# Kernel optimization log

Hardware: AMD Instinct MI355X
Metric: run time of the kernel (lower is better)

## Reference

```python
import jax, jax.numpy as jnp
import numpy as np

B, N, C = 8, 1024, 768
H, D = 12, 64
SCALE = D ** -0.5
EPS = 1e-5

def layernorm(x, g, b):
    mu = jnp.mean(x, axis=-1, keepdims=True)
    var = jnp.var(x, axis=-1, keepdims=True)
    return (x - mu) * jax.lax.rsqrt(var + EPS) * g + b

def setup_inputs() -> dict:
    key = jax.random.key(0)
    ks = jax.random.split(key, 5)
    return {
        "x": jax.random.normal(ks[0], (B, N, C), jnp.float32),
        "qkv_w": jax.random.normal(ks[1], (3 * C, C), jnp.float32) * 0.02,
        "qkv_b": jax.random.normal(ks[2], (3 * C,), jnp.float32) * 0.02,
        "qn_g": jnp.ones((D,), jnp.float32),
        "qn_b": jnp.zeros((D,), jnp.float32),
        "kn_g": jnp.ones((D,), jnp.float32),
        "kn_b": jnp.zeros((D,), jnp.float32),
        "proj_w": jax.random.normal(ks[3], (C, C), jnp.float32) * 0.02,
        "proj_b": jnp.zeros((C,), jnp.float32),
    }

def reference(x, qkv_w, qkv_b, qn_g, qn_b, kn_g, kn_b, proj_w, proj_b):
    # qkv projection: [B,N,3C] -> [3,B,H,N,D]
    qkv = jnp.einsum('bnc,oc->bno', x, qkv_w) + qkv_b
    qkv = qkv.reshape(B, N, 3, H, D).transpose(2, 0, 3, 1, 4)
    q, k, v = qkv[0], qkv[1], qkv[2]
    q = layernorm(q, qn_g, qn_b) * SCALE
    k = layernorm(k, kn_g, kn_b)
    # explicit attention matrix [B,H,N,N] (module stores it)
    attn = jax.nn.softmax(jnp.einsum('bhqd,bhkd->bhqk', q, k), axis=-1)
    out = jnp.einsum('bhqk,bhkd->bhqd', attn, v)
    out = out.transpose(0, 2, 1, 3).reshape(B, N, C)
    out = jnp.einsum('bnc,oc->bno', out, proj_w) + proj_b
    return out
```

## Files before the change

kernel.cpp:

```cpp
#include <hip/hip_runtime.h>
#include <cstdint>

#define Bz 8
#define Nn 1024
#define Cc 768
#define Hh 12
#define Dd 64
#define C3 2304
#define BN 8192

constexpr float EPS = 1e-5f;
constexpr float QSCALE = 0.125f * 1.44269504088896340736f;

typedef __attribute__((ext_vector_type(8))) short bf16x8;
typedef _Float16 f16x8 __attribute__((ext_vector_type(8)));
typedef __attribute__((ext_vector_type(4))) float f32x4;
typedef __attribute__((ext_vector_type(16))) float f32x16;

__device__ __forceinline__ short f2b(float f) {
    union { float f; unsigned u; } x; x.f = f;
    unsigned r = x.u + 0x7FFFu + ((x.u >> 16) & 1u);
    return (short)(r >> 16);
}
__device__ __forceinline__ unsigned cvtpk(float a, float b) {
    unsigned r;
    asm("v_cvt_pk_bf16_f32 %0, %1, %2" : "=v"(r) : "v"(a), "v"(b));
    return r;
}

__device__ __forceinline__ f32x4 MFMAH(f16x8 a, f16x8 b, f32x4 c) {
    return __builtin_amdgcn_mfma_f32_16x16x32_f16(a, b, c, 0, 0, 0);
}
__device__ __forceinline__ f32x16 MFMA32(bf16x8 a, bf16x8 b, f32x16 c) {
    return __builtin_amdgcn_mfma_f32_32x32x16_bf16(a, b, c, 0, 0, 0);
}
__device__ __forceinline__ f16x8 ldf16(const _Float16* p) { return *(const f16x8*)p; }
__device__ __forceinline__ void gld16(const void* g, void* l) {
    __builtin_amdgcn_global_load_lds((const __attribute__((address_space(1))) unsigned int*)g,
                                     (__attribute__((address_space(3))) unsigned int*)(l),
                                     16, 0, 0);
}

__global__ __launch_bounds__(256) void cvt_all(
    const float* __restrict__ x, const float* __restrict__ wq, const float* __restrict__ wp,
    _Float16* __restrict__ xh, _Float16* __restrict__ wqh, _Float16* __restrict__ wph)
{
    const int n1 = BN * Cc / 8, n2 = n1 + C3 * Cc / 8, n3 = n2 + Cc * Cc / 8;
    int i = blockIdx.x * 256 + threadIdx.x;
    const float* s; _Float16* d; int off;
    if (i < n1)      { s = x;  d = xh;  off = i; }
    else if (i < n2) { s = wq; d = wqh; off = i - n1; }
    else if (i < n3) { s = wp; d = wph; off = i - n2; }
    else return;
    float4 a = *(const float4*)(s + (size_t)off * 8);
    float4 b = *(const float4*)(s + (size_t)off * 8 + 4);
    f16x8 o;
    o[0] = (_Float16)a.x; o[1] = (_Float16)a.y; o[2] = (_Float16)a.z; o[3] = (_Float16)a.w;
    o[4] = (_Float16)b.x; o[5] = (_Float16)b.y; o[6] = (_Float16)b.z; o[7] = (_Float16)b.w;
    *(f16x8*)(d + (size_t)off * 8) = o;
}

template<int EPI>
__global__ __launch_bounds__(256, 2) void gemm_f16(
    const _Float16* __restrict__ A,
    const _Float16* __restrict__ W,
    const float* __restrict__ bias,
    float* __restrict__ Out,
    short* __restrict__ qp, short* __restrict__ kp, short* __restrict__ vp,
    const float* __restrict__ qg, const float* __restrict__ qb,
    const float* __restrict__ kg, const float* __restrict__ kb,
    int nx)
{
    __shared__ _Float16 As[2][128 * 64];
    __shared__ _Float16 Bs[2][128 * 64];
    const int tid = threadIdx.x;
    const int lane = tid & 63;
    const int w = tid >> 6;
    const int wr = w >> 1, wc = w & 1;
    const int l15 = lane & 15, l4 = lane >> 4;
    const int lr = lane >> 3;
    const int lslot = lane & 7;

    {
    }
    const int chunk = gridDim.x >> 3;
    const int wg = (blockIdx.x & 7) * chunk + (blockIdx.x >> 3);
    const int by = wg / nx;
    int bx = wg % nx;
    if (by & 1) bx = nx - 1 - bx;
    const int m0 = by * 128;
    const int n0 = bx * 128;

    auto stage = [&](int kt, int buf) {
        const int k0 = kt * 64;
#pragma unroll
        for (int j = 0; j < 8; ++j) {
            int i = w * 8 + j;
            int isA = (i < 16);
            int ib = isA ? i : i - 16;
            int row = ib * 8 + lr;
            int gslot = lslot ^ (row & 7);
            const _Float16* src = (isA ? A + (size_t)(m0 + row) * 768
                                       : W + (size_t)(n0 + row) * 768) + k0 + gslot * 8;
            _Float16* dst = (isA ? &As[buf][0] : &Bs[buf][0]) + ib * 512;
            gld16(src, dst);
        }
    };

    f32x4 acc[4][4];
#pragma unroll
    for (int mi = 0; mi < 4; ++mi)
#pragma unroll
        for (int ni = 0; ni < 4; ++ni) { acc[mi][ni][0]=0.f; acc[mi][ni][1]=0.f; acc[mi][ni][2]=0.f; acc[mi][ni][3]=0.f; }

    stage(0, 0);
    __syncthreads();

    for (int kt = 0; kt < 12; ++kt) {
        const int cur = kt & 1;
        if (kt < 11) stage(kt + 1, cur ^ 1);
#pragma unroll
        for (int ks = 0; ks < 2; ++ks) {
            f16x8 af[4], bfr[4];
#pragma unroll
            for (int mi = 0; mi < 4; ++mi) {
                int row = wr * 64 + mi * 16 + l15;
                int slot = (ks * 4 + l4) ^ (row & 7);
                af[mi] = ldf16(&As[cur][row * 64 + slot * 8]);
            }
#pragma unroll
            for (int ni = 0; ni < 4; ++ni) {
                int row = wc * 64 + ni * 16 + l15;
                int slot = (ks * 4 + l4) ^ (row & 7);
                bfr[ni] = ldf16(&Bs[cur][row * 64 + slot * 8]);
            }
#pragma unroll
            for (int mi = 0; mi < 4; ++mi)
#pragma unroll
                for (int ni = 0; ni < 4; ++ni)
                    acc[mi][ni] = MFMAH(af[mi], bfr[ni], acc[mi][ni]);
        }
        __syncthreads();
    }

    if (EPI == 0) {
#pragma unroll
        for (int mi = 0; mi < 4; ++mi)
#pragma unroll
            for (int r = 0; r < 4; ++r) {
                int row = m0 + wr * 64 + mi * 16 + l4 * 4 + r;
#pragma unroll
                for (int ni = 0; ni < 4; ++ni) {
                    int col = n0 + wc * 64 + ni * 16 + l15;
                    Out[(size_t)row * Cc + col] = acc[mi][ni][r] + bias[col];
                }
            }
    } else {
        const int ncol0 = n0 + wc * 64;
        const int type = ncol0 / Cc;
        const int h = (ncol0 % Cc) >> 6;
        const float* gptr = (type == 0) ? qg : kg;
        const float* bptr = (type == 0) ? qb : kb;
        float biasv[4], gv[4], bv[4];
#pragma unroll
        for (int ni = 0; ni < 4; ++ni) {
            int d = ni * 16 + l15;
            biasv[ni] = bias[ncol0 + d];
            if (type < 2) { gv[ni] = gptr[d]; bv[ni] = bptr[d]; }
        }
        short* plane = (type == 0) ? qp : (type == 1) ? kp : vp;
#pragma unroll
        for (int mi = 0; mi < 4; ++mi)
#pragma unroll
            for (int r = 0; r < 4; ++r) {
                float v[4];
#pragma unroll
                for (int ni = 0; ni < 4; ++ni) v[ni] = acc[mi][ni][r] + biasv[ni];
                int row = m0 + wr * 64 + mi * 16 + l4 * 4 + r;
                size_t base = ((size_t)row * Hh + h) * 64;
                if (type < 2) {
                    float s = v[0] + v[1] + v[2] + v[3];
#pragma unroll
                    for (int off = 1; off < 16; off <<= 1) s += __shfl_xor(s, off);
                    float mu = s * (1.0f / 64.0f);
                    float s2 = 0.f;
#pragma unroll
                    for (int ni = 0; ni < 4; ++ni) { float dv = v[ni] - mu; s2 += dv * dv; }
#pragma unroll
                    for (int off = 1; off < 16; off <<= 1) s2 += __shfl_xor(s2, off);
                    float inv = rsqrtf(s2 * (1.0f / 64.0f) + EPS);
#pragma unroll
                    for (int ni = 0; ni < 4; ++ni) {
                        float rr = (v[ni] - mu) * inv * gv[ni] + bv[ni];
                        if (type == 0) rr *= QSCALE;
                        plane[base + ni * 16 + l15] = f2b(rr);
                    }
                } else {
#pragma unroll
                    for (int ni = 0; ni < 4; ++ni)
                        plane[base + ni * 16 + l15] = f2b(v[ni]);
                }
            }
    }
}

__global__ __launch_bounds__(256, 4) void flash_attn_mfma(
    const short* __restrict__ qp, const short* __restrict__ kp, const short* __restrict__ vp,
    _Float16* __restrict__ att)
{
    __shared__ short kls[2][64 * 64];
    __shared__ short vtl[2][64 * 64];
    const int tid = threadIdx.x;
    const int lane = tid & 63;
    const int w = tid >> 6;
    const int l31 = lane & 31;
    const int hi = lane >> 5;
    const int lr = lane >> 3;
    const int lslot = lane & 7;
    const int bid = (blockIdx.x & 7) * 96 + (blockIdx.x >> 3);
    const int qt = bid & 7;
    const int bh = bid >> 3;
    const int h = bh % Hh;
    const int b = bh / Hh;
    const int q0 = qt * 128;
    const size_t hbase = ((size_t)b * Nn * Hh + h) * 64;
    const int n0v = (tid & 31) * 2, d0v = (tid >> 5) * 8;

    bf16x8 qf[4];
    {
        const short* qsrc = qp + hbase + (size_t)(q0 + w * 32 + l31) * 768 + hi * 8;
#pragma unroll
        for (int ds = 0; ds < 4; ++ds)
            qf[ds] = *(const bf16x8*)(qsrc + ds * 16);
    }

#pragma unroll
    for (int i = 0; i < 2; ++i) {
        int rl = i * 32 + w * 8 + lr;
        gld16(kp + hbase + (size_t)rl * 768 + (lslot ^ lr) * 8,
              &kls[0][(i * 32 + w * 8) * 64]);
    }
    {
        const short* s0 = vp + hbase + (size_t)n0v * 768 + d0v;
        bf16x8 a0 = *(const bf16x8*)s0;
        bf16x8 a1 = *(const bf16x8*)(s0 + 768);
#pragma unroll
        for (int j = 0; j < 8; ++j) {
            int d = d0v + j;
            unsigned pk = (unsigned short)a0[j] | ((unsigned)(unsigned short)a1[j] << 16);
            *(unsigned*)&vtl[0][d * 64 + (((n0v >> 3) ^ (d & 7)) << 3) + (n0v & 7)] = pk;
        }
    }
    __syncthreads();

    f32x16 o0, o1;
#pragma unroll
    for (int i = 0; i < 16; ++i) { o0[i] = 0.f; o1[i] = 0.f; }
    float lrun = 0.f;
    unsigned afu[4][4];

    for (int kt = 0; kt < 16; ++kt) {
        const int cur = kt & 1, nxt = cur ^ 1;
        bf16x8 va0, va1;
        if (kt < 15) {
#pragma unroll
            for (int i = 0; i < 2; ++i) {
                int rl = i * 32 + w * 8 + lr;
                gld16(kp + hbase + (size_t)((kt + 1) * 64 + rl) * 768 + (lslot ^ lr) * 8,
                      &kls[nxt][(i * 32 + w * 8) * 64]);
            }
            const short* s0 = vp + hbase + (size_t)((kt + 1) * 64 + n0v) * 768 + d0v;
            va0 = *(const bf16x8*)s0;
            va1 = *(const bf16x8*)(s0 + 768);
        }
#pragma unroll
        for (int t2 = 0; t2 < 2; ++t2) {
            f32x16 st;
#pragma unroll
            for (int i = 0; i < 16; ++i) st[i] = 0.f;
            const int row = t2 * 32 + l31;
            const int rsw = row & 7;
#pragma unroll
            for (int ds = 0; ds < 4; ++ds) {
                bf16x8 kf = *(const bf16x8*)&kls[cur][row * 64 + (((ds * 2 + hi) ^ rsw) << 3)];
                st = MFMA32(kf, qf[ds], st);
            }
#pragma unroll
            for (int i = 0; i < 16; ++i) { st[i] = exp2f(st[i]); lrun += st[i]; }
            unsigned pk[8], sx[8];
#pragma unroll
            for (int i = 0; i < 8; ++i) pk[i] = cvtpk(st[2 * i], st[2 * i + 1]);
#pragma unroll
            for (int i = 0; i < 8; ++i) sx[i] = (unsigned)__shfl_xor((int)pk[i], 32);
            afu[t2 * 2 + 0][0] = hi ? sx[2] : pk[0];
            afu[t2 * 2 + 0][1] = hi ? sx[3] : pk[1];
            afu[t2 * 2 + 0][2] = hi ? pk[2] : sx[0];
            afu[t2 * 2 + 0][3] = hi ? pk[3] : sx[1];
            afu[t2 * 2 + 1][0] = hi ? sx[6] : pk[4];
            afu[t2 * 2 + 1][1] = hi ? sx[7] : pk[5];
            afu[t2 * 2 + 1][2] = hi ? pk[6] : sx[4];
            afu[t2 * 2 + 1][3] = hi ? pk[7] : sx[5];
        }
        __builtin_amdgcn_s_setprio(1);
#pragma unroll
        for (int c = 0; c < 4; ++c) {
            union { bf16x8 v; unsigned u[4]; } a;
            a.u[0] = afu[c][0]; a.u[1] = afu[c][1]; a.u[2] = afu[c][2]; a.u[3] = afu[c][3];
            const int r0 = l31, r1 = 32 + l31;
            const int sw = l31 & 7;
            bf16x8 vf0 = *(const bf16x8*)&vtl[cur][r0 * 64 + (((c * 2 + hi) ^ sw) << 3)];
            bf16x8 vf1 = *(const bf16x8*)&vtl[cur][r1 * 64 + (((c * 2 + hi) ^ sw) << 3)];
            o0 = MFMA32(a.v, vf0, o0);
            o1 = MFMA32(a.v, vf1, o1);
        }
        __builtin_amdgcn_s_setprio(0);
        if (kt < 15) {
#pragma unroll
            for (int j = 0; j < 8; ++j) {
                int d = d0v + j;
                unsigned pk = (unsigned short)va0[j] | ((unsigned)(unsigned short)va1[j] << 16);
                *(unsigned*)&vtl[nxt][d * 64 + (((n0v >> 3) ^ (d & 7)) << 3) + (n0v & 7)] = pk;
            }
        }
        __syncthreads();
    }

    lrun += __shfl_xor(lrun, 32);
    float linv = 1.0f / lrun;
#pragma unroll
    for (int r = 0; r < 16; ++r) {
        int qr = (r & 3) + 8 * (r >> 2) + 4 * hi;
        float invr = __shfl(linv, qr);
        int row = q0 + w * 32 + qr;
        _Float16* dst = att + (size_t)(b * Nn + row) * Cc + h * 64 + l31;
        dst[0]  = (_Float16)(o0[r] * invr);
        dst[32] = (_Float16)(o1[r] * invr);
    }
}

extern "C" void kernel_launch(void* const* d_in, const int* in_sizes, int n_in,
                              void* d_out, int out_size, void* d_ws, size_t ws_size,
                              hipStream_t stream)
{
    const float* x      = (const float*)d_in[0];
    const float* qkv_w  = (const float*)d_in[1];
    const float* qkv_b  = (const float*)d_in[2];
    const float* qn_g   = (const float*)d_in[3];
    const float* qn_b   = (const float*)d_in[4];
    const float* kn_g   = (const float*)d_in[5];
    const float* kn_b   = (const float*)d_in[6];
    const float* proj_w = (const float*)d_in[7];
    const float* proj_b = (const float*)d_in[8];
    float* out = (float*)d_out;

    char* ws = (char*)d_ws;
    short*    qp  = (short*)(ws);
    short*    kp  = (short*)(ws + 12582912);
    short*    vp  = (short*)(ws + 25165824);
    _Float16* att = (_Float16*)(ws + 37748736);
    _Float16* xh  = (_Float16*)(ws + 50331648);
    _Float16* wqh = (_Float16*)(ws + 62914560);
    _Float16* wph = (_Float16*)(ws + 66453504);

    {
        const int n3 = BN * Cc / 8 + C3 * Cc / 8 + Cc * Cc / 8;
        cvt_all<<<(n3 + 255) / 256, 256, 0, stream>>>(x, qkv_w, proj_w, xh, wqh, wph);
    }
    gemm_f16<1><<<(BN / 128) * (C3 / 128), 256, 0, stream>>>(
        xh, wqh, qkv_b, nullptr, qp, kp, vp, qn_g, qn_b, kn_g, kn_b, C3 / 128);
    flash_attn_mfma<<<Bz * Hh * 8, 256, 0, stream>>>(qp, kp, vp, att);
    gemm_f16<0><<<(BN / 128) * (Cc / 128), 256, 0, stream>>>(
        att, wph, proj_b, out, nullptr, nullptr, nullptr, nullptr, nullptr, nullptr, nullptr, Cc / 128);
}
```

Measured before the change: 128.0 us.

## Shrink flash-attention blocks to 2 waves and 32-key tiles with new swizzle

The attention kernel now runs 128-thread blocks, each covering 64 query rows, and launches twice as many blocks. Keys and values are streamed in 32-row tiles instead of 64. Because each key tile now fits a single 32x32 MFMA, the cross-half shuffle that rebuilt the P operand is gone, and V gets a new transposed LDS layout with a different XOR swizzle. This is meant to raise occupancy and drop shuffle overhead, at the cost of each block loading K/V twice as often per query and hitting the barrier more times.

```diff
diff --git a/kernel.cpp b/kernel.cpp
--- a/kernel.cpp
+++ b/kernel.cpp
@@ -81,8 +81,6 @@
     const int lr = lane >> 3;
     const int lslot = lane & 7;
 
-    {
-    }
     const int chunk = gridDim.x >> 3;
     const int wg = (blockIdx.x & 7) * chunk + (blockIdx.x >> 3);
     const int by = wg / nx;
@@ -204,12 +202,12 @@
     }
 }
 
-__global__ __launch_bounds__(256, 4) void flash_attn_mfma(
+__global__ __launch_bounds__(128, 4) void flash_attn_mfma(
     const short* __restrict__ qp, const short* __restrict__ kp, const short* __restrict__ vp,
     _Float16* __restrict__ att)
 {
-    __shared__ short kls[2][64 * 64];
-    __shared__ short vtl[2][64 * 64];
+    __shared__ short kls[2][32 * 64];
+    __shared__ short vtl[2][64 * 32];
     const int tid = threadIdx.x;
     const int lane = tid & 63;
     const int w = tid >> 6;
@@ -217,14 +215,15 @@
     const int hi = lane >> 5;
     const int lr = lane >> 3;
     const int lslot = lane & 7;
-    const int bid = (blockIdx.x & 7) * 96 + (blockIdx.x >> 3);
-    const int qt = bid & 7;
-    const int bh = bid >> 3;
+    const int bid = (blockIdx.x & 7) * 192 + (blockIdx.x >> 3);
+    const int qt = bid & 15;
+    const int bh = bid >> 4;
     const int h = bh % Hh;
     const int b = bh / Hh;
-    const int q0 = qt * 128;
+    const int q0 = qt * 64;
     const size_t hbase = ((size_t)b * Nn * Hh + h) * 64;
-    const int n0v = (tid & 31) * 2, d0v = (tid >> 5) * 8;
+    const int n0v = (tid & 15) * 2, d0v = (tid >> 4) * 8;
+    const int ksw = n0v ^ (((((n0v >> 2) ^ (n0v >> 3)) & 1)) * 12);
 
     bf16x8 qf[4];
     {
@@ -234,22 +233,25 @@
             qf[ds] = *(const bf16x8*)(qsrc + ds * 16);
     }
 
+    auto vcommit = [&](int buf, bf16x8 a0, bf16x8 a1) {
+#pragma unroll
+        for (int j = 0; j < 8; ++j) {
+            int d = d0v + j;
+            int swd = (d ^ (d >> 2)) & 3;
+            unsigned pk_ = (unsigned short)a0[j] | ((unsigned)(unsigned short)a1[j] << 16);
+            *(unsigned*)&vtl[buf][d * 32 + ((((ksw >> 3) ^ swd)) << 3) + (ksw & 7)] = pk_;
+        }
+    };
+
 #pragma unroll
     for (int i = 0; i < 2; ++i) {
-        int rl = i * 32 + w * 8 + lr;
-        gld16(kp + hbase + (size_t)rl * 768 + (lslot ^ lr) * 8,
-              &kls[0][(i * 32 + w * 8) * 64]);
+        int row = w * 16 + i * 8 + lr;
+        gld16(kp + hbase + (size_t)row * 768 + (lslot ^ lr) * 8,
+              &kls[0][(w * 16 + i * 8) * 64]);
     }
     {
         const short* s0 = vp + hbase + (size_t)n0v * 768 + d0v;
-        bf16x8 a0 = *(const bf16x8*)s0;
-        bf16x8 a1 = *(const bf16x8*)(s0 + 768);
-#pragma unroll
-        for (int j = 0; j < 8; ++j) {
-            int d = d0v + j;
-            unsigned pk = (unsigned short)a0[j] | ((unsigned)(unsigned short)a1[j] << 16);
-            *(unsigned*)&vtl[0][d * 64 + (((n0v >> 3) ^ (d & 7)) << 3) + (n0v & 7)] = pk;
-        }
+        vcommit(0, *(const bf16x8*)s0, *(const bf16x8*)(s0 + 768));
     }
     __syncthreads();
 
@@ -257,71 +259,60 @@
 #pragma unroll
     for (int i = 0; i < 16; ++i) { o0[i] = 0.f; o1[i] = 0.f; }
     float lrun = 0.f;
-    unsigned afu[4][4];
-
-    for (int kt = 0; kt < 16; ++kt) {
+
+    for (int kt = 0; kt < 32; ++kt) {
         const int cur = kt & 1, nxt = cur ^ 1;
         bf16x8 va0, va1;
-        if (kt < 15) {
+        if (kt < 31) {
 #pragma unroll
             for (int i = 0; i < 2; ++i) {
-                int rl = i * 32 + w * 8 + lr;
-                gld16(kp + hbase + (size_t)((kt + 1) * 64 + rl) * 768 + (lslot ^ lr) * 8,
-                      &kls[nxt][(i * 32 + w * 8) * 64]);
-            }
-            const short* s0 = vp + hbase + (size_t)((kt + 1) * 64 + n0v) * 768 + d0v;
+                int row = w * 16 + i * 8 + lr;
+                gld16(kp + hbase + (size_t)((kt + 1) * 32 + row) * 768 + (lslot ^ lr) * 8,
+                      &kls[nxt][(w * 16 + i * 8) * 64]);
+            }
+            const short* s0 = vp + hbase + (size_t)((kt + 1) * 32 + n0v) * 768 + d0v;
             va0 = *(const bf16x8*)s0;
             va1 = *(const bf16x8*)(s0 + 768);
         }
-#pragma unroll
-        for (int t2 = 0; t2 < 2; ++t2) {
-            f32x16 st;
-#pragma unroll
-            for (int i = 0; i < 16; ++i) st[i] = 0.f;
-            const int row = t2 * 32 + l31;
-            const int rsw = row & 7;
-#pragma unroll
-            for (int ds = 0; ds < 4; ++ds) {
-                bf16x8 kf = *(const bf16x8*)&kls[cur][row * 64 + (((ds * 2 + hi) ^ rsw) << 3)];
-                st = MFMA32(kf, qf[ds], st);
-            }
-#pragma unroll
-            for (int i = 0; i < 16; ++i) { st[i] = exp2f(st[i]); lrun += st[i]; }
-            unsigned pk[8], sx[8];
-#pragma unroll
-            for (int i = 0; i < 8; ++i) pk[i] = cvtpk(st[2 * i], st[2 * i + 1]);
-#pragma unroll
-            for (int i = 0; i < 8; ++i) sx[i] = (unsigned)__shfl_xor((int)pk[i], 32);
-            afu[t2 * 2 + 0][0] = hi ? sx[2] : pk[0];
-            afu[t2 * 2 + 0][1] = hi ? sx[3] : pk[1];
-            afu[t2 * 2 + 0][2] = hi ? pk[2] : sx[0];
-            afu[t2 * 2 + 0][3] = hi ? pk[3] : sx[1];
-            afu[t2 * 2 + 1][0] = hi ? sx[6] : pk[4];
-            afu[t2 * 2 + 1][1] = hi ? sx[7] : pk[5];
-            afu[t2 * 2 + 1][2] = hi ? pk[6] : sx[4];
-            afu[t2 * 2 + 1][3] = hi ? pk[7] : sx[5];
-        }
+        f32x16 st;
+#pragma unroll
+        for (int i = 0; i < 16; ++i) st[i] = 0.f;
         __builtin_amdgcn_s_setprio(1);
 #pragma unroll
-        for (int c = 0; c < 4; ++c) {
+        for (int ds = 0; ds < 4; ++ds) {
+            bf16x8 kf = *(const bf16x8*)&kls[cur][l31 * 64 + (((ds * 2 + hi) ^ (l31 & 7)) << 3)];
+            st = MFMA32(kf, qf[ds], st);
+        }
+        __builtin_amdgcn_s_setprio(0);
+#pragma unroll
+        for (int i = 0; i < 16; ++i) st[i] = exp2f(st[i]);
+        {
+            float s01 = (st[0] + st[1]) + (st[2] + st[3]);
+            float s23 = (st[4] + st[5]) + (st[6] + st[7]);
+            float s45 = (st[8] + st[9]) + (st[10] + st[11]);
+            float s67 = (st[12] + st[13]) + (st[14] + st[15]);
+            lrun += (s01 + s23) + (s45 + s67);
+        }
+        unsigned pk[8];
+#pragma unroll
+        for (int i = 0; i < 8; ++i) pk[i] = cvtpk(st[2 * i], st[2 * i + 1]);
+        __builtin_amdgcn_s_setprio(1);
+#pragma unroll
+        for (int c = 0; c < 2; ++c) {
             union { bf16x8 v; unsigned u[4]; } a;
-            a.u[0] = afu[c][0]; a.u[1] = afu[c][1]; a.u[2] = afu[c][2]; a.u[3] = afu[c][3];
-            const int r0 = l31, r1 = 32 + l31;
-            const int sw = l31 & 7;
-            bf16x8 vf0 = *(const bf16x8*)&vtl[cur][r0 * 64 + (((c * 2 + hi) ^ sw) << 3)];
-            bf16x8 vf1 = *(const bf16x8*)&vtl[cur][r1 * 64 + (((c * 2 + hi) ^ sw) << 3)];
-            o0 = MFMA32(a.v, vf0, o0);
-            o1 = MFMA32(a.v, vf1, o1);
+            a.u[0] = pk[c * 4 + 0]; a.u[1] = pk[c * 4 + 1];
+            a.u[2] = pk[c * 4 + 2]; a.u[3] = pk[c * 4 + 3];
+#pragma unroll
+            for (int nt = 0; nt < 2; ++nt) {
+                int r = nt * 32 + l31;
+                int swd = (r ^ (r >> 2)) & 3;
+                bf16x8 vf = *(const bf16x8*)&vtl[cur][r * 32 + (((c * 2 + hi) ^ swd) << 3)];
+                if (nt == 0) o0 = MFMA32(a.v, vf, o0);
+                else         o1 = MFMA32(a.v, vf, o1);
+            }
         }
         __builtin_amdgcn_s_setprio(0);
-        if (kt < 15) {
-#pragma unroll
-            for (int j = 0; j < 8; ++j) {
-                int d = d0v + j;
-                unsigned pk = (unsigned short)va0[j] | ((unsigned)(unsigned short)va1[j] << 16);
-                *(unsigned*)&vtl[nxt][d * 64 + (((n0v >> 3) ^ (d & 7)) << 3) + (n0v & 7)] = pk;
-            }
-        }
+        if (kt < 31) vcommit(nxt, va0, va1);
         __syncthreads();
     }
 
@@ -368,7 +359,7 @@
     }
     gemm_f16<1><<<(BN / 128) * (C3 / 128), 256, 0, stream>>>(
         xh, wqh, qkv_b, nullptr, qp, kp, vp, qn_g, qn_b, kn_g, kn_b, C3 / 128);
-    flash_attn_mfma<<<Bz * Hh * 8, 256, 0, stream>>>(qp, kp, vp, att);
+    flash_attn_mfma<<<Bz * Hh * 16, 128, 0, stream>>>(qp, kp, vp, att);
     gemm_f16<0><<<(BN / 128) * (Cc / 128), 256, 0, stream>>>(
         att, wph, proj_b, out, nullptr, nullptr, nullptr, nullptr, nullptr, nullptr, nullptr, Cc / 128);
 }
```

Result: slower. 135.8 us (+6.0%).
